# Kernel optimization log

Hardware: AMD Instinct MI355X
Metric: run time of the kernel (lower is better)

Reference implementation:

```python
import jax, jax.numpy as jnp
import numpy as np

D_MODEL = 1024
NUM_HEADS = 16
D_K = D_MODEL // NUM_HEADS
ROPE_THETA = 10000.0


def apply_rope(x, pos):
    # x: [B, nh, S, d_k], pos: [S]
    d = x.shape[-1]
    inv_freq = ROPE_THETA ** (-jnp.arange(0, d, 2, dtype=jnp.float32) / d)  # [d/2]
    ang = pos.astype(jnp.float32)[:, None] * inv_freq[None, :]              # [S, d/2]
    cos, sin = jnp.cos(ang), jnp.sin(ang)
    x1, x2 = x[..., 0::2], x[..., 1::2]
    out_even = x1 * cos - x2 * sin
    out_odd = x1 * sin + x2 * cos
    return jnp.stack([out_even, out_odd], axis=-1).reshape(x.shape)


def setup_inputs() -> dict:
    key = jax.random.key(0)
    kx, kq, kk, kv, ko = jax.random.split(key, 5)
    B, S = 4, 2048
    std = np.sqrt(2.0 / (D_MODEL + D_MODEL))
    x = jax.random.normal(kx, (B, S, D_MODEL), dtype=jnp.float32)
    q_proj = jax.random.normal(kq, (D_MODEL, D_MODEL), dtype=jnp.float32) * std
    k_proj = jax.random.normal(kk, (D_MODEL, D_MODEL), dtype=jnp.float32) * std
    v_proj = jax.random.normal(kv, (D_MODEL, D_MODEL), dtype=jnp.float32) * std
    o_proj = jax.random.normal(ko, (D_MODEL, D_MODEL), dtype=jnp.float32) * std
    return {"x": x, "q_proj": q_proj, "k_proj": k_proj, "v_proj": v_proj, "o_proj": o_proj}


def reference(x, q_proj, k_proj, v_proj, o_proj):
    B, S, D = x.shape
    nh, dk = NUM_HEADS, D // NUM_HEADS
    # projections: weights stored [d_out, d_in] -> x @ W.T
    def split_heads(t):
        return t.reshape(B, S, nh, dk).transpose(0, 2, 1, 3)  # [B, nh, S, dk]
    q = split_heads(x @ q_proj.T)
    k = split_heads(x @ k_proj.T)
    v = split_heads(x @ v_proj.T)
    pos = jnp.arange(S)
    q = apply_rope(q, pos)
    k = apply_rope(k, pos)
    scores = jnp.einsum('bhqd,bhkd->bhqk', q, k) / jnp.sqrt(jnp.float32(dk))
    causal = jnp.tril(jnp.ones((S, S), dtype=bool))
    scores = jnp.where(causal, scores, -jnp.inf)
    attn = jax.nn.softmax(scores, axis=-1)
    out = jnp.einsum('bhqk,bhkd->bhqd', attn, v)          # [B, nh, S, dk]
    out = out.transpose(0, 2, 1, 3).reshape(B, S, D)      # merge heads
    return out @ o_proj.T
```

## Files before the change

kernel.cpp:

```cpp
#include <hip/hip_runtime.h>
#include <hip/hip_bf16.h>
#include <cstdint>


typedef __attribute__((ext_vector_type(8))) short short8;
typedef __attribute__((ext_vector_type(4))) float float4v;

#define MFMA16(a, b, c) __builtin_amdgcn_mfma_f32_16x16x32_bf16((a), (b), (c), 0, 0, 0)

__device__ __forceinline__ void glds16(const void* g, void* l) {
    __builtin_amdgcn_global_load_lds(
        (const __attribute__((address_space(1))) void*)g,
        (__attribute__((address_space(3))) void*)l, 16, 0, 0);
}

__device__ __forceinline__ unsigned int pk2(float a, float b) {
    __hip_bfloat162 h = __float22bfloat162_rn(make_float2(a, b));
    union { __hip_bfloat162 h; unsigned int u; } v; v.h = h;
    return v.u;
}

__device__ __forceinline__ unsigned short f2bf(float x) {
    union { float f; unsigned int u; } v; v.f = x;
    unsigned int r = (v.u + 0x7FFFu + ((v.u >> 16) & 1u)) >> 16;
    return (unsigned short)r;
}

__device__ __forceinline__ float bf2f(unsigned short b) {
    union { unsigned int u; float f; } v; v.u = ((unsigned int)b) << 16;
    return v.f;
}

__device__ __forceinline__ short8 load8f(const float* p) {
    const float4 f0 = *(const float4*)p;
    const float4 f1 = *(const float4*)(p + 4);
    union { short8 s; unsigned int u[4]; } r;
    r.u[0] = pk2(f0.x, f0.y);
    r.u[1] = pk2(f0.z, f0.w);
    r.u[2] = pk2(f1.x, f1.y);
    r.u[3] = pk2(f1.z, f1.w);
    return r.s;
}

__global__ __launch_bounds__(256) void convert_x_table(
    const float* __restrict__ in, __hip_bfloat16* __restrict__ out,
    float2* __restrict__ table)
{
    if (blockIdx.x < 4096) {
        const int idx = (blockIdx.x * 256 + threadIdx.x) * 8;
        *(short8*)(out + idx) = load8f(in + idx);
    } else {
        const int idx = (blockIdx.x - 4096) * 256 + threadIdx.x;
        const int pos = idx >> 5, fi = idx & 31;
        const float f = exp2f(-(float)fi * (13.287712379549449f / 32.0f));
        float sn, cs;
        sincosf((float)pos * f, &sn, &cs);
        table[idx] = make_float2(cs, sn);
    }
}

__global__ __launch_bounds__(256) void convert4_kernel(
    const float* __restrict__ a, const float* __restrict__ b,
    const float* __restrict__ c, const float* __restrict__ d,
    __hip_bfloat16* __restrict__ oa, __hip_bfloat16* __restrict__ ob,
    __hip_bfloat16* __restrict__ oc, __hip_bfloat16* __restrict__ od)
{
    const int m = blockIdx.x >> 9;
    const float* in = (m == 0) ? a : (m == 1) ? b : (m == 2) ? c : d;
    __hip_bfloat16* out = (m == 0) ? oa : (m == 1) ? ob : (m == 2) ? oc : od;
    const int idx = ((blockIdx.x & 511) * 256 + threadIdx.x) * 8;
    *(short8*)(out + idx) = load8f(in + idx);
}

template<int BBF>
__global__ __launch_bounds__(256) void qkv_gemm(
    const __hip_bfloat16* __restrict__ Abf,
    const void* __restrict__ Wq, const void* __restrict__ Wk, const void* __restrict__ Wv,
    __hip_bfloat16* __restrict__ Qp, __hip_bfloat16* __restrict__ Kp,
    __hip_bfloat16* __restrict__ Vt, const float2* __restrict__ table)
{
    __shared__ unsigned short smem[12288];

    const int K = 1024;
    const int bm = blockIdx.x / 48, bn = blockIdx.x % 48;
    const int widx = bn >> 4;
    const int bcol0 = (bn & 15) * 64;
    const void* W = (widx == 0) ? Wq : (widx == 1) ? Wk : Wv;

    const int tid = threadIdx.x;
    const int wave = tid >> 6, lane = tid & 63;
    const int wm = (wave >> 1) * 64, wn = (wave & 1) * 32;
    const int m16 = lane & 15, quad = lane >> 4;

    const int grow = lane >> 3;
    const int gcolsw = ((lane & 7) ^ (lane >> 3)) * 8;
    const int srow = tid >> 3, scol = (tid & 7) * 8;

    float4v acc[4][2] = {};

    for (int k0 = 0; k0 < K; k0 += 64) {
        short8 rb[2];
        if (!BBF) {
            const float* Wf = (const float*)W;
#pragma unroll
            for (int t = 0; t < 2; t++)
                rb[t] = load8f(Wf + (int64_t)(bcol0 + t * 32 + srow) * K + k0 + scol);
        }
        __syncthreads();
        {
            const __hip_bfloat16* g = Abf + (int64_t)(bm * 128 + wave * 32 + grow) * K + k0 + gcolsw;
#pragma unroll
            for (int t = 0; t < 4; t++)
                glds16(g + (int64_t)(t * 8) * K, &smem[(wave * 32 + t * 8) * 64]);
        }
        if (BBF) {
            const __hip_bfloat16* g = (const __hip_bfloat16*)W +
                (int64_t)(bcol0 + wave * 16 + grow) * K + k0 + gcolsw;
#pragma unroll
            for (int t = 0; t < 2; t++)
                glds16(g + (int64_t)(t * 8) * K, &smem[8192 + (wave * 16 + t * 8) * 64]);
        } else {
#pragma unroll
            for (int t = 0; t < 2; t++) {
                const int r = t * 32 + srow;
                *(short8*)&smem[8192 + r * 64 + (scol ^ ((r & 7) * 8))] = rb[t];
            }
        }
        __syncthreads();

#pragma unroll
        for (int kk = 0; kk < 2; kk++) {
            const int ksw = (kk * 32 + quad * 8) ^ ((m16 & 7) * 8);
            short8 af[4], bf[2];
#pragma unroll
            for (int i = 0; i < 4; i++)
                af[i] = *(const short8*)&smem[(wm + i * 16 + m16) * 64 + ksw];
#pragma unroll
            for (int j = 0; j < 2; j++)
                bf[j] = *(const short8*)&smem[8192 + (wn + j * 16 + m16) * 64 + ksw];
#pragma unroll
            for (int i = 0; i < 4; i++)
#pragma unroll
                for (int j = 0; j < 2; j++)
                    acc[i][j] = MFMA16(af[i], bf[j], acc[i][j]);
        }
    }

    if (widx == 2) {
        __syncthreads();
#pragma unroll
        for (int i = 0; i < 4; i++)
#pragma unroll
            for (int j = 0; j < 2; j++) {
                const int col = wn + j * 16 + m16;
                const int key = (col & 7) * 8;
#pragma unroll
                for (int r = 0; r < 4; r++) {
                    const int row = wm + i * 16 + quad * 4 + r;
                    smem[col * 128 + (row ^ key)] = f2bf(acc[i][j][r]);
                }
            }
        __syncthreads();
        const int dc = tid >> 4;
        const int seg = (tid & 15) * 8;
#pragma unroll
        for (int pass = 0; pass < 4; pass++) {
            const int dcol = pass * 16 + dc;
            const short8 v = *(const short8*)&smem[dcol * 128 + (seg ^ ((dcol & 7) * 8))];
            *(short8*)((unsigned short*)Vt + (int64_t)(bcol0 + dcol) * 8192 + bm * 128 + seg) = v;
        }
    } else {
        __hip_bfloat16* dst = (widx == 0) ? Qp : Kp;
        const float scale = (widx == 0) ? 0.18033688011112042f : 1.0f;
        const float sgn = (m16 & 1) ? 1.0f : -1.0f;
        const int row0 = bm * 128 + wm + quad * 4;
        const int col0 = bcol0 + wn + m16;
#pragma unroll
        for (int i = 0; i < 4; i++)
#pragma unroll
            for (int j = 0; j < 2; j++) {
                const int ifq = ((wn + j * 16 + m16) & 63) >> 1;
#pragma unroll
                for (int r = 0; r < 4; r++) {
                    const float v = acc[i][j][r] * scale;
                    const float vp = __shfl_xor(v, 1);
                    const int row = row0 + i * 16 + r;
                    const float2 cs = table[(row & 2047) * 32 + ifq];
                    const float out = v * cs.x + sgn * vp * cs.y;
                    dst[(int64_t)row * 1024 + col0 + j * 16] = __float2bfloat16(out);
                }
            }
    }
}

template<int BBF>
__global__ __launch_bounds__(256) void gemm_o(
    const __hip_bfloat16* __restrict__ Abf, const void* __restrict__ B,
    float* __restrict__ C, int M, int N, int K)
{
    __shared__ __hip_bfloat16 lA[128 * 64];
    __shared__ __hip_bfloat16 lB[64 * 64];

    const int nb = N >> 6;
    const int bm = blockIdx.x / nb, bn = blockIdx.x % nb;
    const int tid = threadIdx.x;
    const int wave = tid >> 6, lane = tid & 63;
    const int wm = (wave >> 1) * 64, wn = (wave & 1) * 32;
    const int m16 = lane & 15, quad = lane >> 4;
    const int grow = lane >> 3;
    const int gcolsw = ((lane & 7) ^ (lane >> 3)) * 8;
    const int srow = tid >> 3, scol = (tid & 7) * 8;

    float4v acc[4][2] = {};

    for (int k0 = 0; k0 < K; k0 += 64) {
        short8 rb[2];
        if (!BBF) {
            const float* Bf = (const float*)B;
#pragma unroll
            for (int t = 0; t < 2; t++)
                rb[t] = load8f(Bf + (int64_t)(bn * 64 + t * 32 + srow) * K + k0 + scol);
        }
        __syncthreads();
        {
            const __hip_bfloat16* g = Abf + (int64_t)(bm * 128 + wave * 32 + grow) * K + k0 + gcolsw;
#pragma unroll
            for (int t = 0; t < 4; t++)
                glds16(g + (int64_t)(t * 8) * K, &lA[(wave * 32 + t * 8) * 64]);
        }
        if (BBF) {
            const __hip_bfloat16* g = (const __hip_bfloat16*)B +
                (int64_t)(bn * 64 + wave * 16 + grow) * K + k0 + gcolsw;
#pragma unroll
            for (int t = 0; t < 2; t++)
                glds16(g + (int64_t)(t * 8) * K, &lB[(wave * 16 + t * 8) * 64]);
        } else {
#pragma unroll
            for (int t = 0; t < 2; t++) {
                const int r = t * 32 + srow;
                *(short8*)&lB[r * 64 + (scol ^ ((r & 7) * 8))] = rb[t];
            }
        }
        __syncthreads();

#pragma unroll
        for (int kk = 0; kk < 2; kk++) {
            const int ksw = (kk * 32 + quad * 8) ^ ((m16 & 7) * 8);
            short8 af[4], bf[2];
#pragma unroll
            for (int i = 0; i < 4; i++)
                af[i] = *(const short8*)&lA[(wm + i * 16 + m16) * 64 + ksw];
#pragma unroll
            for (int j = 0; j < 2; j++)
                bf[j] = *(const short8*)&lB[(wn + j * 16 + m16) * 64 + ksw];
#pragma unroll
            for (int i = 0; i < 4; i++)
#pragma unroll
                for (int j = 0; j < 2; j++)
                    acc[i][j] = MFMA16(af[i], bf[j], acc[i][j]);
        }
    }

    const int row0 = bm * 128 + wm + quad * 4;
    const int col0 = bn * 64 + wn + m16;
#pragma unroll
    for (int i = 0; i < 4; i++)
#pragma unroll
        for (int j = 0; j < 2; j++)
#pragma unroll
            for (int r = 0; r < 4; r++)
                C[(int64_t)(row0 + i * 16 + r) * N + col0 + j * 16] = acc[i][j][r];
}

__global__ __launch_bounds__(256) void attn_kernel(
    const __hip_bfloat16* __restrict__ Q,
    const __hip_bfloat16* __restrict__ Kg,
    const __hip_bfloat16* __restrict__ Vt,
    __hip_bfloat16* __restrict__ O,
    int S, int BS)
{
    const int g = blockIdx.x >> 6;
    const int qt = (g < 4) ? 15 - g : (g < 8) ? 11 - g : (g < 12) ? g : g - 12;
    const int bh = blockIdx.x & 63;
    const int b = bh >> 4, h = bh & 15;
    const int tid = threadIdx.x;
    const int wave = tid >> 6, lane = tid & 63;
    const int m16 = lane & 15, quad = lane >> 4;

    __shared__ __hip_bfloat16 lK[64 * 64];
    __shared__ __hip_bfloat16 lV[64 * 64];
    __shared__ __hip_bfloat16 lP[4][32 * 64];

    const int qrow0 = qt * 128 + wave * 32;
    const int64_t rowbase = (int64_t)b * S;

    short8 aq[2][2];
#pragma unroll
    for (int i = 0; i < 2; i++) {
        const __hip_bfloat16* qp = Q + (rowbase + qrow0 + i * 16 + m16) * 1024 + h * 64 + quad * 8;
        aq[i][0] = *(const short8*)qp;
        aq[i][1] = *(const short8*)(qp + 32);
    }

    float lsum[2] = {0.f, 0.f};
    float4v o_acc[2][4] = {};

    const int srow = tid >> 3;
    const int scol = (tid & 7) * 8;

    const int ktmax_blk = 2 * qt + 1;
    const int ktmax_w = 2 * qt + (wave >> 1);
    const int k8 = (m16 & 7) * 8;

    short8 pk0, pk1, pv0, pv1;
#define PREFETCH(KT)                                                                          \
    do {                                                                                      \
        pk0 = *(const short8*)(Kg + (rowbase + (KT) * 64 + srow) * 1024 + h * 64 + scol);     \
        pk1 = *(const short8*)(Kg + (rowbase + (KT) * 64 + srow + 32) * 1024 + h * 64 + scol);\
        pv0 = *(const short8*)(Vt + (int64_t)(h * 64 + srow) * BS + rowbase + (KT) * 64 + scol);      \
        pv1 = *(const short8*)(Vt + (int64_t)(h * 64 + srow + 32) * BS + rowbase + (KT) * 64 + scol); \
    } while (0)

    PREFETCH(0);

    for (int kt = 0; kt <= ktmax_blk; kt++) {
        __syncthreads();
        *(short8*)&lK[srow * 64 + (scol ^ ((srow & 7) * 8))] = pk0;
        *(short8*)&lK[(srow + 32) * 64 + (scol ^ (((srow + 32) & 7) * 8))] = pk1;
        *(short8*)&lV[srow * 64 + (scol ^ ((srow & 7) * 8))] = pv0;
        *(short8*)&lV[(srow + 32) * 64 + (scol ^ (((srow + 32) & 7) * 8))] = pv1;
        __syncthreads();

        if (kt < ktmax_blk) PREFETCH(kt + 1);

        if (kt <= ktmax_w) {
            float4v st[4][2] = {};
#pragma unroll
            for (int mi = 0; mi < 4; mi++) {
                const int n = mi * 16 + m16;
                const int sw = (n & 7) * 8;
                short8 k0 = *(const short8*)&lK[n * 64 + ((quad * 8) ^ sw)];
                short8 k1 = *(const short8*)&lK[n * 64 + ((32 + quad * 8) ^ sw)];
#pragma unroll
                for (int ni = 0; ni < 2; ni++) {
                    st[mi][ni] = MFMA16(k0, aq[ni][0], st[mi][ni]);
                    st[mi][ni] = MFMA16(k1, aq[ni][1], st[mi][ni]);
                }
            }

            const bool need_mask = (kt * 64 + 63 > qrow0);
#pragma unroll
            for (int ni = 0; ni < 2; ni++) {
                const int qg = qrow0 + ni * 16 + m16;
#pragma unroll
                for (int mi = 0; mi < 4; mi++) {
                    float p[4];
#pragma unroll
                    for (int r = 0; r < 4; r++) {
                        p[r] = __builtin_amdgcn_exp2f(st[mi][ni][r]);
                        if (need_mask) {
                            const int kvg = kt * 64 + mi * 16 + quad * 4 + r;
                            if (kvg > qg) p[r] = 0.0f;
                        }
                    }
                    lsum[ni] += (p[0] + p[1]) + (p[2] + p[3]);
                    uint2 w;
                    w.x = pk2(p[0], p[1]);
                    w.y = pk2(p[2], p[3]);
                    *(uint2*)&lP[wave][(ni * 16 + m16) * 64 + ((mi * 16 + quad * 4) ^ k8)] = w;
                }
            }

            short8 ap[2][2];
#pragma unroll
            for (int i = 0; i < 2; i++)
#pragma unroll
                for (int ks = 0; ks < 2; ks++)
                    ap[i][ks] = *(const short8*)
                        &lP[wave][(i * 16 + m16) * 64 + ((ks * 32 + quad * 8) ^ k8)];
#pragma unroll
            for (int jd = 0; jd < 4; jd++) {
                const int d = jd * 16 + m16;
                const int sw = (d & 7) * 8;
                short8 b0 = *(const short8*)&lV[d * 64 + ((quad * 8) ^ sw)];
                short8 b1 = *(const short8*)&lV[d * 64 + ((32 + quad * 8) ^ sw)];
#pragma unroll
                for (int i = 0; i < 2; i++) {
                    o_acc[i][jd] = MFMA16(ap[i][0], b0, o_acc[i][jd]);
                    o_acc[i][jd] = MFMA16(ap[i][1], b1, o_acc[i][jd]);
                }
            }
        }
    }
#undef PREFETCH

    float rinv[2];
#pragma unroll
    for (int ni = 0; ni < 2; ni++) {
        float v = lsum[ni];
        v += __shfl_xor(v, 16);
        v += __shfl_xor(v, 32);
        rinv[ni] = 1.0f / v;
    }
    float ri[2][4];
#pragma unroll
    for (int i = 0; i < 2; i++)
#pragma unroll
        for (int r = 0; r < 4; r++)
            ri[i][r] = __shfl(rinv[i], quad * 4 + r);

#pragma unroll
    for (int i = 0; i < 2; i++)
#pragma unroll
        for (int jd = 0; jd < 4; jd++)
#pragma unroll
            for (int r = 0; r < 4; r++) {
                const int row = qrow0 + i * 16 + quad * 4 + r;
                O[(rowbase + row) * 1024 + h * 64 + jd * 16 + m16] =
                    __float2bfloat16(o_acc[i][jd][r] * ri[i][r]);
            }
}

extern "C" void kernel_launch(void* const* d_in, const int* in_sizes, int n_in,
                              void* d_out, int out_size, void* d_ws, size_t ws_size,
                              hipStream_t stream)
{
    const float* x  = (const float*)d_in[0];
    const float* qw = (const float*)d_in[1];
    const float* kw = (const float*)d_in[2];
    const float* vw = (const float*)d_in[3];
    const float* ow = (const float*)d_in[4];

    const int BS = 8192, D = 1024, S = 2048;
    const size_t MiB = 1024 * 1024;

    char* ws = (char*)d_ws;
    __hip_bfloat16* xb  = (__hip_bfloat16*)(ws);
    __hip_bfloat16* Qb  = (__hip_bfloat16*)(ws + 16 * MiB);
    __hip_bfloat16* Kb  = (__hip_bfloat16*)(ws + 32 * MiB);
    __hip_bfloat16* Vtb = (__hip_bfloat16*)(ws + 48 * MiB);
    __hip_bfloat16* wqb = (__hip_bfloat16*)(ws + 64 * MiB);
    __hip_bfloat16* wkb = (__hip_bfloat16*)(ws + 66 * MiB);
    __hip_bfloat16* wvb = (__hip_bfloat16*)(ws + 68 * MiB);
    __hip_bfloat16* wob = (__hip_bfloat16*)(ws + 70 * MiB);
    float2* table = (float2*)((char*)d_out + 31 * MiB);
    const bool wbf = ws_size >= 72 * MiB;

    dim3 blk(256);
    convert_x_table<<<4096 + 256, blk, 0, stream>>>(x, xb, table);
    if (wbf) {
        convert4_kernel<<<4 * (D * D) / 2048, blk, 0, stream>>>(
            qw, kw, vw, ow, wqb, wkb, wvb, wob);
        qkv_gemm<1><<<64 * 48, blk, 0, stream>>>(xb, wqb, wkb, wvb, Qb, Kb, Vtb, table);
    } else {
        qkv_gemm<0><<<64 * 48, blk, 0, stream>>>(xb, qw, kw, vw, Qb, Kb, Vtb, table);
    }
    attn_kernel<<<4 * 16 * (S / 128), blk, 0, stream>>>(Qb, Kb, Vtb, Qb , S, BS);
    if (wbf) gemm_o<1><<<(BS / 128) * (D / 64), blk, 0, stream>>>(Qb, wob, (float*)d_out, BS, D, D);
    else     gemm_o<0><<<(BS / 128) * (D / 64), blk, 0, stream>>>(Qb, ow,  (float*)d_out, BS, D, D);
}
```

Before: 250.6 us.

## Overlap next-tile LDS loads with MFMA in bf16 GEMMs and merge convert kernels

In the bf16-weight path of the QKV and output GEMMs, the main loop is restructured so the global-to-LDS load for the next K tile is issued once the second-half fragments have been read into registers. Those MFMAs then run while the load is in flight, partly hiding load latency with a single LDS buffer. The x conversion, weight conversion and RoPE table kernels are also merged into one launch to cut a kernel launch and its tail. The single-buffer scheme depends on the barrier placement being right.

```diff
diff --git a/kernel.cpp b/kernel.cpp
--- a/kernel.cpp
+++ b/kernel.cpp
@@ -40,6 +40,34 @@
     r.u[2] = pk2(f1.x, f1.y);
     r.u[3] = pk2(f1.z, f1.w);
     return r.s;
+}
+
+__global__ __launch_bounds__(256) void convert_all(
+    const float* __restrict__ x, __hip_bfloat16* __restrict__ xb,
+    const float* __restrict__ a, const float* __restrict__ b,
+    const float* __restrict__ c, const float* __restrict__ d,
+    __hip_bfloat16* __restrict__ oa, __hip_bfloat16* __restrict__ ob,
+    __hip_bfloat16* __restrict__ oc, __hip_bfloat16* __restrict__ od,
+    float2* __restrict__ table)
+{
+    const int bid = blockIdx.x;
+    if (bid < 4096) {
+        const int idx = (bid * 256 + threadIdx.x) * 8;
+        *(short8*)(xb + idx) = load8f(x + idx);
+    } else if (bid < 6144) {
+        const int m = (bid - 4096) >> 9;
+        const float* in = (m == 0) ? a : (m == 1) ? b : (m == 2) ? c : d;
+        __hip_bfloat16* out = (m == 0) ? oa : (m == 1) ? ob : (m == 2) ? oc : od;
+        const int idx = (((bid - 4096) & 511) * 256 + threadIdx.x) * 8;
+        *(short8*)(out + idx) = load8f(in + idx);
+    } else {
+        const int idx = (bid - 6144) * 256 + threadIdx.x;
+        const int pos = idx >> 5, fi = idx & 31;
+        const float f = exp2f(-(float)fi * (13.287712379549449f / 32.0f));
+        float sn, cs;
+        sincosf((float)pos * f, &sn, &cs);
+        table[idx] = make_float2(cs, sn);
+    }
 }
 
 __global__ __launch_bounds__(256) void convert_x_table(
@@ -59,19 +87,6 @@
     }
 }
 
-__global__ __launch_bounds__(256) void convert4_kernel(
-    const float* __restrict__ a, const float* __restrict__ b,
-    const float* __restrict__ c, const float* __restrict__ d,
-    __hip_bfloat16* __restrict__ oa, __hip_bfloat16* __restrict__ ob,
-    __hip_bfloat16* __restrict__ oc, __hip_bfloat16* __restrict__ od)
-{
-    const int m = blockIdx.x >> 9;
-    const float* in = (m == 0) ? a : (m == 1) ? b : (m == 2) ? c : d;
-    __hip_bfloat16* out = (m == 0) ? oa : (m == 1) ? ob : (m == 2) ? oc : od;
-    const int idx = ((blockIdx.x & 511) * 256 + threadIdx.x) * 8;
-    *(short8*)(out + idx) = load8f(in + idx);
-}
-
 template<int BBF>
 __global__ __launch_bounds__(256) void qkv_gemm(
     const __hip_bfloat16* __restrict__ Abf,
@@ -98,51 +113,91 @@
 
     float4v acc[4][2] = {};
 
-    for (int k0 = 0; k0 < K; k0 += 64) {
-        short8 rb[2];
-        if (!BBF) {
+    if (BBF) {
+        const __hip_bfloat16* ga = Abf + (int64_t)(bm * 128 + wave * 32 + grow) * K + gcolsw;
+        const __hip_bfloat16* gb = (const __hip_bfloat16*)W +
+                                   (int64_t)(bcol0 + wave * 16 + grow) * K + gcolsw;
+#define QSTG(KOFF)                                                              \
+        do {                                                                    \
+            glds16(ga + (KOFF),                   &smem[(wave * 32 +  0) * 64]);\
+            glds16(ga + (KOFF) + (int64_t)8 * K,  &smem[(wave * 32 +  8) * 64]);\
+            glds16(ga + (KOFF) + (int64_t)16 * K, &smem[(wave * 32 + 16) * 64]);\
+            glds16(ga + (KOFF) + (int64_t)24 * K, &smem[(wave * 32 + 24) * 64]);\
+            glds16(gb + (KOFF),                   &smem[8192 + (wave * 16 + 0) * 64]);\
+            glds16(gb + (KOFF) + (int64_t)8 * K,  &smem[8192 + (wave * 16 + 8) * 64]);\
+        } while (0)
+        QSTG(0);
+        for (int k0 = 0; k0 < K; k0 += 64) {
+            __syncthreads();
+            short8 af[4], bf[2];
+            {
+                const int ksw = (quad * 8) ^ ((m16 & 7) * 8);
+#pragma unroll
+                for (int i = 0; i < 4; i++)
+                    af[i] = *(const short8*)&smem[(wm + i * 16 + m16) * 64 + ksw];
+#pragma unroll
+                for (int j = 0; j < 2; j++)
+                    bf[j] = *(const short8*)&smem[8192 + (wn + j * 16 + m16) * 64 + ksw];
+#pragma unroll
+                for (int i = 0; i < 4; i++)
+#pragma unroll
+                    for (int j = 0; j < 2; j++)
+                        acc[i][j] = MFMA16(af[i], bf[j], acc[i][j]);
+            }
+            {
+                const int ksw = (32 + quad * 8) ^ ((m16 & 7) * 8);
+#pragma unroll
+                for (int i = 0; i < 4; i++)
+                    af[i] = *(const short8*)&smem[(wm + i * 16 + m16) * 64 + ksw];
+#pragma unroll
+                for (int j = 0; j < 2; j++)
+                    bf[j] = *(const short8*)&smem[8192 + (wn + j * 16 + m16) * 64 + ksw];
+            }
+            __syncthreads();
+            if (k0 + 64 < K) QSTG(k0 + 64);
+#pragma unroll
+            for (int i = 0; i < 4; i++)
+#pragma unroll
+                for (int j = 0; j < 2; j++)
+                    acc[i][j] = MFMA16(af[i], bf[j], acc[i][j]);
+        }
+#undef QSTG
+    } else {
+        for (int k0 = 0; k0 < K; k0 += 64) {
+            short8 rb[2];
             const float* Wf = (const float*)W;
 #pragma unroll
             for (int t = 0; t < 2; t++)
                 rb[t] = load8f(Wf + (int64_t)(bcol0 + t * 32 + srow) * K + k0 + scol);
-        }
-        __syncthreads();
-        {
-            const __hip_bfloat16* g = Abf + (int64_t)(bm * 128 + wave * 32 + grow) * K + k0 + gcolsw;
-#pragma unroll
-            for (int t = 0; t < 4; t++)
-                glds16(g + (int64_t)(t * 8) * K, &smem[(wave * 32 + t * 8) * 64]);
-        }
-        if (BBF) {
-            const __hip_bfloat16* g = (const __hip_bfloat16*)W +
-                (int64_t)(bcol0 + wave * 16 + grow) * K + k0 + gcolsw;
-#pragma unroll
-            for (int t = 0; t < 2; t++)
-                glds16(g + (int64_t)(t * 8) * K, &smem[8192 + (wave * 16 + t * 8) * 64]);
-        } else {
+            __syncthreads();
+            {
+                const __hip_bfloat16* g = Abf + (int64_t)(bm * 128 + wave * 32 + grow) * K + k0 + gcolsw;
+#pragma unroll
+                for (int t = 0; t < 4; t++)
+                    glds16(g + (int64_t)(t * 8) * K, &smem[(wave * 32 + t * 8) * 64]);
+            }
 #pragma unroll
             for (int t = 0; t < 2; t++) {
                 const int r = t * 32 + srow;
                 *(short8*)&smem[8192 + r * 64 + (scol ^ ((r & 7) * 8))] = rb[t];
             }
-        }
-        __syncthreads();
-
-#pragma unroll
-        for (int kk = 0; kk < 2; kk++) {
-            const int ksw = (kk * 32 + quad * 8) ^ ((m16 & 7) * 8);
-            short8 af[4], bf[2];
-#pragma unroll
-            for (int i = 0; i < 4; i++)
-                af[i] = *(const short8*)&smem[(wm + i * 16 + m16) * 64 + ksw];
-#pragma unroll
-            for (int j = 0; j < 2; j++)
-                bf[j] = *(const short8*)&smem[8192 + (wn + j * 16 + m16) * 64 + ksw];
-#pragma unroll
-            for (int i = 0; i < 4; i++)
-#pragma unroll
-                for (int j = 0; j < 2; j++)
-                    acc[i][j] = MFMA16(af[i], bf[j], acc[i][j]);
+            __syncthreads();
+#pragma unroll
+            for (int kk = 0; kk < 2; kk++) {
+                const int ksw = (kk * 32 + quad * 8) ^ ((m16 & 7) * 8);
+                short8 af[4], bf[2];
+#pragma unroll
+                for (int i = 0; i < 4; i++)
+                    af[i] = *(const short8*)&smem[(wm + i * 16 + m16) * 64 + ksw];
+#pragma unroll
+                for (int j = 0; j < 2; j++)
+                    bf[j] = *(const short8*)&smem[8192 + (wn + j * 16 + m16) * 64 + ksw];
+#pragma unroll
+                for (int i = 0; i < 4; i++)
+#pragma unroll
+                    for (int j = 0; j < 2; j++)
+                        acc[i][j] = MFMA16(af[i], bf[j], acc[i][j]);
+            }
         }
     }
 
@@ -213,51 +268,91 @@
 
     float4v acc[4][2] = {};
 
-    for (int k0 = 0; k0 < K; k0 += 64) {
-        short8 rb[2];
-        if (!BBF) {
+    if (BBF) {
+        const __hip_bfloat16* ga = Abf + (int64_t)(bm * 128 + wave * 32 + grow) * K + gcolsw;
+        const __hip_bfloat16* gb = (const __hip_bfloat16*)B +
+                                   (int64_t)(bn * 64 + wave * 16 + grow) * K + gcolsw;
+#define OSTG(KOFF)                                                              \
+        do {                                                                    \
+            glds16(ga + (KOFF),                   &lA[(wave * 32 +  0) * 64]);  \
+            glds16(ga + (KOFF) + (int64_t)8 * K,  &lA[(wave * 32 +  8) * 64]);  \
+            glds16(ga + (KOFF) + (int64_t)16 * K, &lA[(wave * 32 + 16) * 64]);  \
+            glds16(ga + (KOFF) + (int64_t)24 * K, &lA[(wave * 32 + 24) * 64]);  \
+            glds16(gb + (KOFF),                   &lB[(wave * 16 + 0) * 64]);   \
+            glds16(gb + (KOFF) + (int64_t)8 * K,  &lB[(wave * 16 + 8) * 64]);   \
+        } while (0)
+        OSTG(0);
+        for (int k0 = 0; k0 < K; k0 += 64) {
+            __syncthreads();
+            short8 af[4], bf[2];
+            {
+                const int ksw = (quad * 8) ^ ((m16 & 7) * 8);
+#pragma unroll
+                for (int i = 0; i < 4; i++)
+                    af[i] = *(const short8*)&lA[(wm + i * 16 + m16) * 64 + ksw];
+#pragma unroll
+                for (int j = 0; j < 2; j++)
+                    bf[j] = *(const short8*)&lB[(wn + j * 16 + m16) * 64 + ksw];
+#pragma unroll
+                for (int i = 0; i < 4; i++)
+#pragma unroll
+                    for (int j = 0; j < 2; j++)
+                        acc[i][j] = MFMA16(af[i], bf[j], acc[i][j]);
+            }
+            {
+                const int ksw = (32 + quad * 8) ^ ((m16 & 7) * 8);
+#pragma unroll
+                for (int i = 0; i < 4; i++)
+                    af[i] = *(const short8*)&lA[(wm + i * 16 + m16) * 64 + ksw];
+#pragma unroll
+                for (int j = 0; j < 2; j++)
+                    bf[j] = *(const short8*)&lB[(wn + j * 16 + m16) * 64 + ksw];
+            }
+            __syncthreads();
+            if (k0 + 64 < K) OSTG(k0 + 64);
+#pragma unroll
+            for (int i = 0; i < 4; i++)
+#pragma unroll
+                for (int j = 0; j < 2; j++)
+                    acc[i][j] = MFMA16(af[i], bf[j], acc[i][j]);
+        }
+#undef OSTG
+    } else {
+        for (int k0 = 0; k0 < K; k0 += 64) {
+            short8 rb[2];
             const float* Bf = (const float*)B;
 #pragma unroll
             for (int t = 0; t < 2; t++)
                 rb[t] = load8f(Bf + (int64_t)(bn * 64 + t * 32 + srow) * K + k0 + scol);
-        }
-        __syncthreads();
-        {
-            const __hip_bfloat16* g = Abf + (int64_t)(bm * 128 + wave * 32 + grow) * K + k0 + gcolsw;
-#pragma unroll
-            for (int t = 0; t < 4; t++)
-                glds16(g + (int64_t)(t * 8) * K, &lA[(wave * 32 + t * 8) * 64]);
-        }
-        if (BBF) {
-            const __hip_bfloat16* g = (const __hip_bfloat16*)B +
-                (int64_t)(bn * 64 + wave * 16 + grow) * K + k0 + gcolsw;
-#pragma unroll
-            for (int t = 0; t < 2; t++)
-                glds16(g + (int64_t)(t * 8) * K, &lB[(wave * 16 + t * 8) * 64]);
-        } else {
+            __syncthreads();
+            {
+                const __hip_bfloat16* g = Abf + (int64_t)(bm * 128 + wave * 32 + grow) * K + k0 + gcolsw;
+#pragma unroll
+                for (int t = 0; t < 4; t++)
+                    glds16(g + (int64_t)(t * 8) * K, &lA[(wave * 32 + t * 8) * 64]);
+            }
 #pragma unroll
             for (int t = 0; t < 2; t++) {
                 const int r = t * 32 + srow;
                 *(short8*)&lB[r * 64 + (scol ^ ((r & 7) * 8))] = rb[t];
             }
-        }
-        __syncthreads();
-
-#pragma unroll
-        for (int kk = 0; kk < 2; kk++) {
-            const int ksw = (kk * 32 + quad * 8) ^ ((m16 & 7) * 8);
-            short8 af[4], bf[2];
-#pragma unroll
-            for (int i = 0; i < 4; i++)
-                af[i] = *(const short8*)&lA[(wm + i * 16 + m16) * 64 + ksw];
-#pragma unroll
-            for (int j = 0; j < 2; j++)
-                bf[j] = *(const short8*)&lB[(wn + j * 16 + m16) * 64 + ksw];
-#pragma unroll
-            for (int i = 0; i < 4; i++)
-#pragma unroll
-                for (int j = 0; j < 2; j++)
-                    acc[i][j] = MFMA16(af[i], bf[j], acc[i][j]);
+            __syncthreads();
+#pragma unroll
+            for (int kk = 0; kk < 2; kk++) {
+                const int ksw = (kk * 32 + quad * 8) ^ ((m16 & 7) * 8);
+                short8 af[4], bf[2];
+#pragma unroll
+                for (int i = 0; i < 4; i++)
+                    af[i] = *(const short8*)&lA[(wm + i * 16 + m16) * 64 + ksw];
+#pragma unroll
+                for (int j = 0; j < 2; j++)
+                    bf[j] = *(const short8*)&lB[(wn + j * 16 + m16) * 64 + ksw];
+#pragma unroll
+                for (int i = 0; i < 4; i++)
+#pragma unroll
+                    for (int j = 0; j < 2; j++)
+                        acc[i][j] = MFMA16(af[i], bf[j], acc[i][j]);
+            }
         }
     }
 
@@ -447,12 +542,12 @@
     const bool wbf = ws_size >= 72 * MiB;
 
     dim3 blk(256);
-    convert_x_table<<<4096 + 256, blk, 0, stream>>>(x, xb, table);
     if (wbf) {
-        convert4_kernel<<<4 * (D * D) / 2048, blk, 0, stream>>>(
-            qw, kw, vw, ow, wqb, wkb, wvb, wob);
+        convert_all<<<4096 + 2048 + 256, blk, 0, stream>>>(
+            x, xb, qw, kw, vw, ow, wqb, wkb, wvb, wob, table);
         qkv_gemm<1><<<64 * 48, blk, 0, stream>>>(xb, wqb, wkb, wvb, Qb, Kb, Vtb, table);
     } else {
+        convert_x_table<<<4096 + 256, blk, 0, stream>>>(x, xb, table);
         qkv_gemm<0><<<64 * 48, blk, 0, stream>>>(xb, qw, kw, vw, Qb, Kb, Vtb, table);
     }
     attn_kernel<<<4 * 16 * (S / 128), blk, 0, stream>>>(Qb, Kb, Vtb, Qb , S, BS);
```

New measurement: 265.8 us. 6.1% more time.
